# Optimization experiments

Measured on AMD Instinct MI355X. Metric: run time of the kernel, lower is better.

The kernel has to match this reference:

```python
import jax, jax.numpy as jnp
import numpy as np

B, S, T, H, F, V, OUT = 32, 40, 60, 256, 64, 50000, 128
D_IN = H + F  # LSTM input = input_size + feature_size (input_size == hidden_size)


def setup_inputs() -> dict:
    rng = np.random.default_rng(0)
    key = jax.random.key(0)
    ks = jax.random.split(key, 12)
    sc = 0.05
    # descending sentence counts per paragraph (pack_padded_sequence order), max == S
    lens = np.sort(rng.integers(1, S + 1, size=B))[::-1].copy()
    lens[0] = S
    # per-sentence token lengths; trailing (padding) sentences have length 0
    tok_len = rng.integers(1, T + 1, size=(B, S))
    tok_len = tok_len * (np.arange(S)[None, :] < lens[:, None])
    x_mask = jnp.asarray(np.arange(T)[None, None, :] >= tok_len[:, :, None])  # True = pad
    return {
        "x": jax.random.randint(ks[0], (B, S, T), 0, V),
        "x_mask": x_mask,
        "x_feature": jax.random.normal(ks[1], (B, S, T, F), jnp.float32),
        "sentences_len": jnp.asarray(lens, jnp.int32),
        "clause": jnp.zeros((B,), jnp.int32),
        "cls": jnp.zeros((B,), jnp.int32),
        "emb": jax.random.normal(ks[2], (V, H), jnp.float32) * 0.02,
        "attn_w": jax.random.normal(ks[3], (H,), jnp.float32) * sc,
        "attn_b": jnp.zeros((), jnp.float32),
        "wih_f": jax.random.normal(ks[4], (4 * H, D_IN), jnp.float32) * sc,
        "whh_f": jax.random.normal(ks[5], (4 * H, H), jnp.float32) * sc,
        "bih_f": jnp.zeros((4 * H,), jnp.float32),
        "bhh_f": jnp.zeros((4 * H,), jnp.float32),
        "wih_b": jax.random.normal(ks[6], (4 * H, D_IN), jnp.float32) * sc,
        "whh_b": jax.random.normal(ks[7], (4 * H, H), jnp.float32) * sc,
        "bih_b": jnp.zeros((4 * H,), jnp.float32),
        "bhh_b": jnp.zeros((4 * H,), jnp.float32),
        "fc_w": jax.random.normal(ks[8], (OUT, 2 * H), jnp.float32) * sc,
        "fc_b": jnp.zeros((OUT,), jnp.float32),
        "bn_gamma": jnp.ones((OUT,), jnp.float32),
        "bn_beta": jnp.zeros((OUT,), jnp.float32),
    }


def _lstm_last(X, m, wih, whh, bih, bhh, reverse):
    # X: (S, B, D) time-major inputs; m: (S, B) bool validity mask.
    # Masked update emulates pack_padded_sequence: carry freezes past each seq's length,
    # so the final carry equals torch's h_n for that direction.
    def step(carry, inp):
        h, c = carry
        xt, mt = inp
        g = xt @ wih.T + bih + h @ whh.T + bhh
        i, f, gg, o = jnp.split(g, 4, axis=-1)  # torch gate order i,f,g,o
        c2 = jax.nn.sigmoid(f) * c + jax.nn.sigmoid(i) * jnp.tanh(gg)
        h2 = jax.nn.sigmoid(o) * jnp.tanh(c2)
        upd = mt[:, None]
        return (jnp.where(upd, h2, h), jnp.where(upd, c2, c)), None

    nb, nh = X.shape[1], whh.shape[1]
    init = (jnp.zeros((nb, nh), X.dtype), jnp.zeros((nb, nh), X.dtype))
    (h, _), _ = jax.lax.scan(step, init, (X, m), reverse=reverse)
    return h


def _forward(x, x_mask, x_feature, sentences_len, emb, attn_w, attn_b,
             wih_f, whh_f, bih_f, bhh_f, wih_b, whh_b, bih_b, bhh_b,
             fc_w, fc_b, bn_gamma, bn_beta):
    e = emb[x]                                            # (B,S,T,H)
    valid_tok = ~x_mask                                   # (B,S,T)
    valid_sen = jnp.any(valid_tok, axis=-1)               # (B,S)
    score = jnp.einsum('bsth,h->bst', e, attn_w) + attn_b
    score = jnp.where(valid_tok, score, -jnp.inf)
    score = jnp.where(valid_sen[..., None], score, 0.0)   # avoid all-inf NaN rows
    alpha = jax.nn.relu(jax.nn.softmax(score, axis=-1))   # (B,S,T)
    alpha = jnp.where(valid_sen[..., None] & valid_tok, alpha, 0.0)
    emb_part = jnp.einsum('bst,bsth->bsh', alpha, e)      # attended sum over tokens
    feat_part = jnp.sum(x_feature * valid_tok[..., None].astype(x_feature.dtype), axis=2)
    sen = jnp.concatenate([emb_part, feat_part], axis=-1) # (B,S,H+F)
    sen = sen * valid_sen[..., None].astype(sen.dtype)    # empty sentences -> zero rows
    X = jnp.transpose(sen, (1, 0, 2))                     # (S,B,H+F) time-major
    m = jnp.arange(X.shape[0])[:, None] < sentences_len[None, :]  # (S,B)
    h_f = _lstm_last(X, m, wih_f, whh_f, bih_f, bhh_f, reverse=False)
    h_b = _lstm_last(X, m, wih_b, whh_b, bih_b, bhh_b, reverse=True)
    # torch: paragraph_hidden[0].view(batch, -1) on (2,B,H) = flat memory reinterpretation
    hidden = jnp.stack([h_f, h_b], axis=0).reshape(x.shape[0], -1)  # (B,2H)
    logits = hidden @ fc_w.T + fc_b                       # (B,OUT)
    mu = jnp.mean(logits, axis=0)
    var = jnp.mean((logits - mu) ** 2, axis=0)            # biased var (BN train mode)
    y = jax.nn.relu(bn_gamma * (logits - mu) / jnp.sqrt(var + 1e-5) + bn_beta)
    return jax.nn.log_softmax(y, axis=0)                  # original softmaxes over batch dim


def reference(x, x_mask, x_feature, sentences_len, clause, cls, emb, attn_w, attn_b,
              wih_f, whh_f, bih_f, bhh_f, wih_b, whh_b, bih_b, bhh_b,
              fc_w, fc_b, bn_gamma, bn_beta):
    # clause / cls are unused by the original forward
    return _forward(x, x_mask, x_feature, sentences_len, emb, attn_w, attn_b,
                    wih_f, whh_f, bih_f, bhh_f, wih_b, whh_b, bih_b, bhh_b,
                    fc_w, fc_b, bn_gamma, bn_beta)
```

## Files before the change

kernel.cpp:

```cpp
#include <hip/hip_runtime.h>
#include <stdint.h>

#define NB 32
#define NS 40
#define NT 60
#define NH 256
#define NF 64
#define NDIN 320
#define NG 1024
#define NSB 1280
#define NOUT 128

typedef __bf16 bf16x8 __attribute__((ext_vector_type(8)));
typedef float f32x4 __attribute__((ext_vector_type(4)));
typedef uint32_t u32x4 __attribute__((ext_vector_type(4)));

union bfrag { bf16x8 v; uint16_t u[8]; uint4 q; uint64_t d[2]; };
union f2arr { float2 v; float a[2]; };

__device__ __forceinline__ uint16_t f2bf(float f) {
  uint32_t u = __float_as_uint(f);
  u += 0x7fffu + ((u >> 16) & 1u);
  return (uint16_t)(u >> 16);
}
__device__ __forceinline__ float bf2f(uint16_t h) {
  return __uint_as_float(((uint32_t)h) << 16);
}
__device__ __forceinline__ float sig_fast(float x) { return 1.0f / (1.0f + __expf(-x)); }
__device__ __forceinline__ float tanh_fast(float x) {
  x = fminf(fmaxf(x, -15.0f), 15.0f);
  float t = __expf(2.0f * x);
  return (t - 1.0f) / (t + 1.0f);
}
__device__ __forceinline__ uint32_t ld_agent_u32(const uint32_t* p) {
  return __hip_atomic_load(p, __ATOMIC_RELAXED, __HIP_MEMORY_SCOPE_AGENT);
}

__global__ __launch_bounds__(256) void k_detect(const uint32_t* __restrict__ xm,
                                                int* __restrict__ flags,
                                                uint32_t* __restrict__ gr) {
  int bid = blockIdx.x, tid = threadIdx.x;
  {
    int gidx = bid * 256 + tid;
    u32x4 z = {0, 0, 0, 0};
    asm volatile("global_store_dwordx4 %0, %1, off sc1"
                 :: "v"((unsigned long long)(uintptr_t)(gr + (size_t)gidx * 4)), "v"(z)
                 : "memory");
  }
  __shared__ int s_notint, s_notflt;
  if (tid == 0) { s_notint = 0; s_notflt = 0; }
  __syncthreads();
  int notint = 0, notflt = 0;
  for (int i = bid * 600 + tid; i < (bid + 1) * 600; i += 256) {
    uint32_t v = xm[i];
    if (v > 1u) notint = 1;
    if (v != 0u && v != 0x3f800000u) notflt = 1;
  }
  if (notint) atomicOr(&s_notint, 1);
  if (notflt) atomicOr(&s_notflt, 1);
  __syncthreads();
  if (tid == 0) flags[8 + bid] = s_notint | (s_notflt << 1);
}

__global__ __launch_bounds__(256) void k_attn_prep(
    const int* __restrict__ x, const void* __restrict__ xmask,
    const float* __restrict__ xfeat, const int* __restrict__ slen,
    const float* __restrict__ emb, const float* __restrict__ attn_w,
    uint16_t* __restrict__ Xb, const int* __restrict__ flagp,
    const float* __restrict__ wf, const float* __restrict__ wb,
    uint16_t* __restrict__ outw)
{
  int tid = threadIdx.x;
  if (blockIdx.x >= 1280) {
    const int n = NG * NDIN;
    for (int idx = (blockIdx.x - 1280) * 256 + tid; idx < 2 * n; idx += 1280 * 256) {
      float v = (idx < n) ? wf[idx] : wb[idx - n];
      uint16_t hi = f2bf(v);
      outw[idx] = hi;
      outw[2 * n + idx] = f2bf(v - bf2f(hi));
    }
    return;
  }
  int bs = blockIdx.x;
  int b = bs / NS, s = bs % NS;
  uint16_t* Xh = Xb + (size_t)(s * NB + b) * NDIN;
  uint16_t* Xl = Xh + (size_t)NSB * NDIN;
  int len = slen[b];
  if (s >= len) {
    for (int i = tid; i < NDIN; i += 256) { Xh[i] = 0; Xl[i] = 0; }
    return;
  }
  __shared__ __attribute__((aligned(16))) float sw[NH];
  __shared__ float salpha[NT];
  __shared__ int sidx[NT];
  __shared__ unsigned char svalid[NT];
  __shared__ __attribute__((aligned(16))) uint16_t es[NT][NH];
  sw[tid] = attn_w[tid];
  int nv = 0;
  #pragma unroll
  for (int q = 0; q < 32; q++) nv |= flagp[8 + q];
  int flag = (!(nv & 1)) ? 0 : ((!(nv & 2)) ? 2 : 1);
  if (tid < NT) {
    int mi = bs * NT + tid;
    sidx[tid] = x[mi];
    int mv;
    if (flag == 1)      mv = ((const unsigned char*)xmask)[mi];
    else if (flag == 2) mv = (((const float*)xmask)[mi] != 0.0f) ? 1 : 0;
    else                mv = ((const int*)xmask)[mi];
    svalid[tid] = (mv == 0) ? 1 : 0;
  }
  __syncthreads();
  int wave = tid >> 6, lane = tid & 63;
  for (int t = wave; t < NT; t += 4) {
    float d = 0.0f;
    if (svalid[t]) {
      const float* er = emb + (size_t)sidx[t] * NH;
      float4 e4 = ((const float4*)er)[lane];
      float4 w4 = ((const float4*)sw)[lane];
      uint16_t* ed = &es[t][lane * 4];
      ed[0] = f2bf(e4.x); ed[1] = f2bf(e4.y); ed[2] = f2bf(e4.z); ed[3] = f2bf(e4.w);
      d = e4.x * w4.x + e4.y * w4.y + e4.z * w4.z + e4.w * w4.w;
      #pragma unroll
      for (int o = 32; o > 0; o >>= 1) d += __shfl_down(d, o);
    }
    if (lane == 0) salpha[t] = d;
  }
  __syncthreads();
  if (tid < 64) {
    int valid = (tid < NT) && svalid[tid];
    float v = valid ? salpha[tid] : -1e30f;
    float m = v;
    #pragma unroll
    for (int o = 32; o > 0; o >>= 1) m = fmaxf(m, __shfl_xor(m, o));
    float e = valid ? expf(v - m) : 0.0f;
    float ssum = e;
    #pragma unroll
    for (int o = 32; o > 0; o >>= 1) ssum += __shfl_xor(ssum, o);
    if (tid < NT) salpha[tid] = e / ssum;
  }
  __syncthreads();
  float acc = 0.0f;
  for (int t = 0; t < NT; t++) {
    float a = salpha[t];
    if (a != 0.0f) acc += a * bf2f(es[t][tid]);
  }
  {
    uint16_t hi = f2bf(acc);
    Xh[tid] = hi; Xl[tid] = f2bf(acc - bf2f(hi));
  }
  if (tid < NF) {
    float fa = 0.0f;
    const float* fp = xfeat + (size_t)bs * NT * NF + tid;
    for (int t = 0; t < NT; t++) if (svalid[t]) fa += fp[t * NF];
    uint16_t hi = f2bf(fa);
    Xh[NH + tid] = hi; Xl[NH + tid] = f2bf(fa - bf2f(hi));
  }
}

__global__ __launch_bounds__(512) void k_gbase(
    const uint16_t* __restrict__ Xb, const uint16_t* __restrict__ wihb,
    const float* __restrict__ bih_f, const float* __restrict__ bhh_f,
    const float* __restrict__ bih_b, const float* __restrict__ bhh_b,
    float* __restrict__ gbase)
{
  const int n = NG * NDIN;
  int wave = threadIdx.x >> 6, lane = threadIdx.x & 63;
  int job = blockIdx.x * 8 + wave;
  int dir = job / 1280;
  int r = job % 1280;
  int nt = r % 64, ms = r / 64;
  int m0 = ms * 64;
  const uint16_t* Wh = wihb + (size_t)dir * n;
  const uint16_t* Wl = Wh + (size_t)2 * n;
  const uint16_t* Ah = Xb;
  const uint16_t* Al = Xb + (size_t)NSB * NDIN;
  int lrow = lane & 15, lk = (lane >> 4) * 8;
  f32x4 acc0 = {0,0,0,0}, acc1 = acc0, acc2 = acc0, acc3 = acc0;
  for (int kk = 0; kk < 10; kk++) {
    int k0 = kk * 32 + lk;
    bfrag bh, bl, ah0, ah1, ah2, ah3, al0, al1, al2, al3;
    bh.q = *(const uint4*)(Wh + (size_t)(nt * 16 + lrow) * NDIN + k0);
    bl.q = *(const uint4*)(Wl + (size_t)(nt * 16 + lrow) * NDIN + k0);
    ah0.q = *(const uint4*)(Ah + (size_t)(m0 +  0 + lrow) * NDIN + k0);
    ah1.q = *(const uint4*)(Ah + (size_t)(m0 + 16 + lrow) * NDIN + k0);
    ah2.q = *(const uint4*)(Ah + (size_t)(m0 + 32 + lrow) * NDIN + k0);
    ah3.q = *(const uint4*)(Ah + (size_t)(m0 + 48 + lrow) * NDIN + k0);
    al0.q = *(const uint4*)(Al + (size_t)(m0 +  0 + lrow) * NDIN + k0);
    al1.q = *(const uint4*)(Al + (size_t)(m0 + 16 + lrow) * NDIN + k0);
    al2.q = *(const uint4*)(Al + (size_t)(m0 + 32 + lrow) * NDIN + k0);
    al3.q = *(const uint4*)(Al + (size_t)(m0 + 48 + lrow) * NDIN + k0);
    acc0 = __builtin_amdgcn_mfma_f32_16x16x32_bf16(ah0.v, bh.v, acc0, 0, 0, 0);
    acc0 = __builtin_amdgcn_mfma_f32_16x16x32_bf16(ah0.v, bl.v, acc0, 0, 0, 0);
    acc0 = __builtin_amdgcn_mfma_f32_16x16x32_bf16(al0.v, bh.v, acc0, 0, 0, 0);
    acc1 = __builtin_amdgcn_mfma_f32_16x16x32_bf16(ah1.v, bh.v, acc1, 0, 0, 0);
    acc1 = __builtin_amdgcn_mfma_f32_16x16x32_bf16(ah1.v, bl.v, acc1, 0, 0, 0);
    acc1 = __builtin_amdgcn_mfma_f32_16x16x32_bf16(al1.v, bh.v, acc1, 0, 0, 0);
    acc2 = __builtin_amdgcn_mfma_f32_16x16x32_bf16(ah2.v, bh.v, acc2, 0, 0, 0);
    acc2 = __builtin_amdgcn_mfma_f32_16x16x32_bf16(ah2.v, bl.v, acc2, 0, 0, 0);
    acc2 = __builtin_amdgcn_mfma_f32_16x16x32_bf16(al2.v, bh.v, acc2, 0, 0, 0);
    acc3 = __builtin_amdgcn_mfma_f32_16x16x32_bf16(ah3.v, bh.v, acc3, 0, 0, 0);
    acc3 = __builtin_amdgcn_mfma_f32_16x16x32_bf16(ah3.v, bl.v, acc3, 0, 0, 0);
    acc3 = __builtin_amdgcn_mfma_f32_16x16x32_bf16(al3.v, bh.v, acc3, 0, 0, 0);
  }
  int col = nt * 16 + lrow;
  float bias = dir ? (bih_b[col] + bhh_b[col]) : (bih_f[col] + bhh_f[col]);
  float* gb = gbase + (size_t)dir * NSB * NG;
  int rb = (lane >> 4) * 4;
  #pragma unroll
  for (int rr = 0; rr < 4; rr++) {
    gb[(size_t)(m0 +  0 + rb + rr) * NG + col] = acc0[rr] + bias;
    gb[(size_t)(m0 + 16 + rb + rr) * NG + col] = acc1[rr] + bias;
    gb[(size_t)(m0 + 32 + rb + rr) * NG + col] = acc2[rr] + bias;
    gb[(size_t)(m0 + 48 + rb + rr) * NG + col] = acc3[rr] + bias;
  }
}

__global__ __launch_bounds__(512, 2) void k_lstm(
    const float* __restrict__ whh_f_, const float* __restrict__ whh_b_,
    const float* __restrict__ gbase, const int* __restrict__ slen,
    uint32_t* __restrict__ gr,
    const float* __restrict__ fc_w, const float* __restrict__ fc_b,
    const float* __restrict__ gamma_, const float* __restrict__ beta_,
    float* __restrict__ outp)
{
  __shared__ __attribute__((aligned(16))) char smem_[65664];
  uint16_t (*hs)[264] = (uint16_t(*)[264])smem_;
  volatile float* tsb = (volatile float*)(smem_ + 16896);

  int wg = blockIdx.x;
  int dir = wg >> 3, p = wg & 7;
  int u0 = p * 32;
  int tid = threadIdx.x, wave = tid >> 6, lane = tid & 63;
  int lrow = lane & 15, lkb = (lane >> 4) * 8;
  const float* Wr = dir ? whh_b_ : whh_f_;
  const float* gb = gbase + (size_t)dir * NSB * NG;
  uint32_t* grd = gr + (size_t)dir * 2 * 64 * NB * 4;

  bfrag wh[8];
  {
    int wr = (lrow >> 2) * 256 + u0 + wave * 4 + (lrow & 3);
    const float* wrow = Wr + (size_t)wr * NH;
    #pragma unroll
    for (int kk = 0; kk < 8; kk++) {
      int k0 = kk * 32 + lkb;
      bfrag th;
      #pragma unroll
      for (int e = 0; e < 8; e++) th.u[e] = f2bf(wrow[k0 + e]);
      wh[kk] = th;
    }
  }
  int beta = lane >> 1;
  int g64 = p * 8 + wave;
  int len = slen[beta];
  uint32_t hprev_hi = 0;
  float c0 = 0.0f, c1 = 0.0f;

  unsigned long long sa[2][4];
  #pragma unroll
  for (int par = 0; par < 2; par++) {
    const uint32_t* gpar = grd + (size_t)par * 64 * NB * 4;
    #pragma unroll
    for (int q = 0; q < 4; q++)
      sa[par][q] = (unsigned long long)(uintptr_t)(gpar + (size_t)(tid + q * 512) * 4);
  }

  for (int i = 0; i < NS; i++) {
    int t = dir ? (NS - 1 - i) : i;
    const float* gptr = gb + ((size_t)t * NB + beta) * NG + u0 + wave * 4 + (lane & 1) * 2;
    f2arr g0, g1, g2, g3;
    g0.v = *(const float2*)(gptr);
    g1.v = *(const float2*)(gptr + 256);
    g2.v = *(const float2*)(gptr + 512);
    g3.v = *(const float2*)(gptr + 768);
    u32x4 v0, v1, v2, v3;
    {
      const unsigned long long* a = sa[i & 1];
      uint32_t need = (uint32_t)i;
      long spins = 0;
      for (;;) {
        asm volatile(
          "global_load_dwordx4 %0, %4, off sc1\n\t"
          "global_load_dwordx4 %1, %5, off sc1\n\t"
          "global_load_dwordx4 %2, %6, off sc1\n\t"
          "global_load_dwordx4 %3, %7, off sc1\n\t"
          "s_waitcnt vmcnt(0)"
          : "=&v"(v0), "=&v"(v1), "=&v"(v2), "=&v"(v3)
          : "v"(a[0]), "v"(a[1]), "v"(a[2]), "v"(a[3])
          : "memory");
        if (v0.x >= need && v1.x >= need && v2.x >= need && v3.x >= need) break;
        if (++spins > (1L << 16)) break;
      }
    }
    __syncthreads();
    #pragma unroll
    for (int q = 0; q < 4; q++) {
      int s = tid + q * 512;
      int gq = s >> 5, bb = s & 31;
      u32x4 vv = (q == 0) ? v0 : (q == 1) ? v1 : (q == 2) ? v2 : v3;
      uint32_t* d = (uint32_t*)(&hs[bb][gq * 4]);
      d[0] = vv.y; d[1] = vv.z;
    }
    __syncthreads();
    f32x4 acc0 = {0,0,0,0}, acc1 = acc0;
    #pragma unroll
    for (int kk = 0; kk < 8; kk++) {
      int k0 = kk * 32 + lkb;
      bfrag ah0, ah1;
      ah0.q = *(const uint4*)(&hs[lrow][k0]);
      ah1.q = *(const uint4*)(&hs[16 + lrow][k0]);
      acc0 = __builtin_amdgcn_mfma_f32_16x16x32_bf16(ah0.v, wh[kk].v, acc0, 0, 0, 0);
      acc1 = __builtin_amdgcn_mfma_f32_16x16x32_bf16(ah1.v, wh[kk].v, acc1, 0, 0, 0);
    }
    volatile float* ts = tsb + wave * 576;
    {
      int colT = lane & 15, rb = (lane >> 4) * 4;
      #pragma unroll
      for (int rr = 0; rr < 4; rr++) {
        ts[(rb + rr) * 18 + colT]      = acc0[rr];
        ts[(16 + rb + rr) * 18 + colT] = acc1[rr];
      }
    }
    int e2 = (lane & 1) * 2;
    float gv00 = ts[beta * 18 + 0 + e2],  gv01 = ts[beta * 18 + 1 + e2];
    float gv10 = ts[beta * 18 + 4 + e2],  gv11 = ts[beta * 18 + 5 + e2];
    float gv20 = ts[beta * 18 + 8 + e2],  gv21 = ts[beta * 18 + 9 + e2];
    float gv30 = ts[beta * 18 + 12 + e2], gv31 = ts[beta * 18 + 13 + e2];
    {
      int upd = (t < len) ? 1 : 0;
      float gi0 = gv00 + g0.a[0], gi1 = gv01 + g0.a[1];
      float gf0 = gv10 + g1.a[0], gf1 = gv11 + g1.a[1];
      float gg0 = gv20 + g2.a[0], gg1 = gv21 + g2.a[1];
      float go0 = gv30 + g3.a[0], go1 = gv31 + g3.a[1];
      float c2a = sig_fast(gf0) * c0 + sig_fast(gi0) * tanh_fast(gg0);
      float c2b = sig_fast(gf1) * c1 + sig_fast(gi1) * tanh_fast(gg1);
      float h2a = sig_fast(go0) * tanh_fast(c2a);
      float h2b = sig_fast(go1) * tanh_fast(c2b);
      c0 = upd ? c2a : c0;
      c1 = upd ? c2b : c1;
      uint32_t hiw;
      if (upd) {
        uint16_t ha = f2bf(h2a), hbb = f2bf(h2b);
        hiw = (uint32_t)ha | ((uint32_t)hbb << 16);
      } else hiw = hprev_hi;
      hprev_hi = hiw;
      uint32_t hiw_p = __shfl_down(hiw, 1);
      if ((lane & 1) == 0) {
        uint32_t* gout = grd + ((size_t)(((i + 1) & 1) * 64 + g64) * NB + beta) * 4;
        u32x4 pv;
        pv.x = (uint32_t)(i + 1); pv.y = hiw; pv.z = hiw_p; pv.w = 0u;
        asm volatile("global_store_dwordx4 %0, %1, off sc1"
                     :: "v"((unsigned long long)(uintptr_t)gout), "v"(pv) : "memory");
      }
    }
  }

  #pragma unroll
  for (int q = 0; q < 8; q++) {
    int s = tid + q * 512;
    int d_ = s >> 11, r2 = s & 2047;
    const uint32_t* ga = gr + ((size_t)d_ * 2 * 2048 + r2) * 4;
    long sp = 0;
    while (ld_agent_u32(ga) < (uint32_t)NS) {
      __builtin_amdgcn_s_sleep(1);
      if (++sp > (1L << 20)) break;
    }
  }
  __syncthreads();
  float* hid = (float*)smem_;
  for (int idx = tid; idx < NB * 512; idx += 512) {
    int bb = idx >> 9, k = idx & 511;
    int bsrc = 2 * (bb & 15) + (k >> 8);
    int hcol = k & 255;
    int dirn = (bb < 16) ? 0 : 1;
    const uint32_t* g = gr + ((size_t)dirn * 2 * 64 * NB + (size_t)(hcol >> 2) * NB + bsrc) * 4;
    uint32_t w = ld_agent_u32(g + 1 + ((hcol >> 1) & 1));
    hid[bb * 513 + k] = bf2f((uint16_t)(w >> ((hcol & 1) * 16)));
  }
  __syncthreads();
  int o = blockIdx.x * 8 + wave;
  int b = lane >> 1, half = lane & 1;
  const float* wrow = fc_w + (size_t)o * 512 + half * 256;
  const float* hrow = &hid[b * 513 + half * 256];
  float part = 0.0f;
  #pragma unroll 8
  for (int j = 0; j < 256; j++) part += wrow[j] * hrow[j];
  part += __shfl_xor(part, 1);
  float y = part + fc_b[o];
  float s2 = y;
  #pragma unroll
  for (int off = 2; off < 64; off <<= 1) s2 += __shfl_xor(s2, off);
  float mu = s2 * (1.0f / 32.0f);
  float d = y - mu;
  float v2 = d * d;
  #pragma unroll
  for (int off = 2; off < 64; off <<= 1) v2 += __shfl_xor(v2, off);
  float var = v2 * (1.0f / 32.0f);
  float gm = gamma_[o], be = beta_[o];
  float inv = 1.0f / sqrtf(var + 1e-5f);
  float yy = fmaxf(gm * (y - mu) * inv + be, 0.0f);
  float m = yy;
  #pragma unroll
  for (int off = 2; off < 64; off <<= 1) m = fmaxf(m, __shfl_xor(m, off));
  float e = expf(yy - m);
  float se = e;
  #pragma unroll
  for (int off = 2; off < 64; off <<= 1) se += __shfl_xor(se, off);
  float lse = m + logf(se);
  if (half == 0) outp[b * NOUT + o] = yy - lse;
}

extern "C" void kernel_launch(void* const* d_in, const int* in_sizes, int n_in,
                              void* d_out, int out_size, void* d_ws, size_t ws_size,
                              hipStream_t stream) {
  (void)in_sizes; (void)n_in; (void)out_size; (void)ws_size;
  const int*   x      = (const int*)  d_in[0];
  const void*  xmask  =               d_in[1];
  const float* xfeat  = (const float*)d_in[2];
  const int*   slen   = (const int*)  d_in[3];
  const float* emb    = (const float*)d_in[6];
  const float* attn_w = (const float*)d_in[7];
  const float* wih_f  = (const float*)d_in[9];
  const float* whh_f  = (const float*)d_in[10];
  const float* bih_f  = (const float*)d_in[11];
  const float* bhh_f  = (const float*)d_in[12];
  const float* wih_b  = (const float*)d_in[13];
  const float* whh_b  = (const float*)d_in[14];
  const float* bih_b  = (const float*)d_in[15];
  const float* bhh_b  = (const float*)d_in[16];
  const float* fc_w   = (const float*)d_in[17];
  const float* fc_b   = (const float*)d_in[18];
  const float* gam    = (const float*)d_in[19];
  const float* bet    = (const float*)d_in[20];

  char* ws = (char*)d_ws;
  int*      flags = (int*)ws;
  uint32_t* gr    = (uint32_t*)(ws + 4096);
  uint16_t* Xb    = (uint16_t*)(ws + 135168);
  uint16_t* wihb  = (uint16_t*)(ws + 1773568);
  float*    gbase = (float*)(ws + 4395008);

  k_detect<<<32, 256, 0, stream>>>((const uint32_t*)xmask, flags, gr);
  k_attn_prep<<<2560, 256, 0, stream>>>(x, xmask, xfeat, slen, emb, attn_w, Xb, flags,
                                        wih_f, wih_b, wihb);
  k_gbase<<<320, 512, 0, stream>>>(Xb, wihb, bih_f, bhh_f, bih_b, bhh_b, gbase);
  k_lstm<<<16, 512, 0, stream>>>(whh_f, whh_b, gbase, slen, gr,
                                 fc_w, fc_b, gam, bet, (float*)d_out);
}
```

Measured before the change: 243.9 us.

## Double-buffer LSTM hidden-state LDS tile and batch final hidden gather loads

Adds a second LDS buffer for the per-step hidden-state tile, alternating by step parity, so the barrier before writing the new h can be dropped. The MFMA reads of one step no longer conflict with the next step's writes. The epilogue's per-element flag polling and scattered 32-bit hidden loads are replaced by one batched spin of eight vector loads per thread that carry both the flags and the data, then unpacked into LDS. This cuts a barrier per recurrent step and many serialized global loads, at the cost of more LDS and registers. Correctness depends on the parity buffering being safe given the barrier that remains after the LDS writes.

Result: faster. 229.4 us (-5.9%).

```diff
diff --git a/kernel.cpp b/kernel.cpp
--- a/kernel.cpp
+++ b/kernel.cpp
@@ -224,8 +224,9 @@
     float* __restrict__ outp)
 {
   __shared__ __attribute__((aligned(16))) char smem_[65664];
-  uint16_t (*hs)[264] = (uint16_t(*)[264])smem_;
-  volatile float* tsb = (volatile float*)(smem_ + 16896);
+  uint16_t (*hs0)[264] = (uint16_t(*)[264])smem_;
+  uint16_t (*hs1)[264] = (uint16_t(*)[264])(smem_ + 16896);
+  volatile float* tsb = (volatile float*)(smem_ + 33792);
 
   int wg = blockIdx.x;
   int dir = wg >> 3, p = wg & 7;
@@ -291,13 +292,13 @@
         if (++spins > (1L << 16)) break;
       }
     }
-    __syncthreads();
+    uint16_t (*hcur)[264] = (i & 1) ? hs1 : hs0;
     #pragma unroll
     for (int q = 0; q < 4; q++) {
       int s = tid + q * 512;
       int gq = s >> 5, bb = s & 31;
       u32x4 vv = (q == 0) ? v0 : (q == 1) ? v1 : (q == 2) ? v2 : v3;
-      uint32_t* d = (uint32_t*)(&hs[bb][gq * 4]);
+      uint32_t* d = (uint32_t*)(&hcur[bb][gq * 4]);
       d[0] = vv.y; d[1] = vv.z;
     }
     __syncthreads();
@@ -306,8 +307,8 @@
     for (int kk = 0; kk < 8; kk++) {
       int k0 = kk * 32 + lkb;
       bfrag ah0, ah1;
-      ah0.q = *(const uint4*)(&hs[lrow][k0]);
-      ah1.q = *(const uint4*)(&hs[16 + lrow][k0]);
+      ah0.q = *(const uint4*)(&hcur[lrow][k0]);
+      ah1.q = *(const uint4*)(&hcur[16 + lrow][k0]);
       acc0 = __builtin_amdgcn_mfma_f32_16x16x32_bf16(ah0.v, wh[kk].v, acc0, 0, 0, 0);
       acc1 = __builtin_amdgcn_mfma_f32_16x16x32_bf16(ah1.v, wh[kk].v, acc1, 0, 0, 0);
     }
@@ -354,27 +355,55 @@
     }
   }
 
+  unsigned long long ea0 = (unsigned long long)(uintptr_t)(gr + (size_t)(tid +    0) * 4);
+  unsigned long long ea1 = (unsigned long long)(uintptr_t)(gr + (size_t)(tid +  512) * 4);
+  unsigned long long ea2 = (unsigned long long)(uintptr_t)(gr + (size_t)(tid + 1024) * 4);
+  unsigned long long ea3 = (unsigned long long)(uintptr_t)(gr + (size_t)(tid + 1536) * 4);
+  unsigned long long ea4 = (unsigned long long)(uintptr_t)(gr + (size_t)(4096 + tid +    0) * 4);
+  unsigned long long ea5 = (unsigned long long)(uintptr_t)(gr + (size_t)(4096 + tid +  512) * 4);
+  unsigned long long ea6 = (unsigned long long)(uintptr_t)(gr + (size_t)(4096 + tid + 1024) * 4);
+  unsigned long long ea7 = (unsigned long long)(uintptr_t)(gr + (size_t)(4096 + tid + 1536) * 4);
+  u32x4 w0, w1, w2, w3, w4, w5, w6, w7;
+  {
+    long spins = 0;
+    for (;;) {
+      asm volatile(
+        "global_load_dwordx4 %0, %8, off sc1\n\t"
+        "global_load_dwordx4 %1, %9, off sc1\n\t"
+        "global_load_dwordx4 %2, %10, off sc1\n\t"
+        "global_load_dwordx4 %3, %11, off sc1\n\t"
+        "global_load_dwordx4 %4, %12, off sc1\n\t"
+        "global_load_dwordx4 %5, %13, off sc1\n\t"
+        "global_load_dwordx4 %6, %14, off sc1\n\t"
+        "global_load_dwordx4 %7, %15, off sc1\n\t"
+        "s_waitcnt vmcnt(0)"
+        : "=&v"(w0), "=&v"(w1), "=&v"(w2), "=&v"(w3),
+          "=&v"(w4), "=&v"(w5), "=&v"(w6), "=&v"(w7)
+        : "v"(ea0), "v"(ea1), "v"(ea2), "v"(ea3),
+          "v"(ea4), "v"(ea5), "v"(ea6), "v"(ea7)
+        : "memory");
+      if (w0.x >= (uint32_t)NS && w1.x >= (uint32_t)NS && w2.x >= (uint32_t)NS &&
+          w3.x >= (uint32_t)NS && w4.x >= (uint32_t)NS && w5.x >= (uint32_t)NS &&
+          w6.x >= (uint32_t)NS && w7.x >= (uint32_t)NS) break;
+      if (++spins > (1L << 20)) break;
+    }
+  }
+  __syncthreads();
+  float* hid = (float*)smem_;
   #pragma unroll
   for (int q = 0; q < 8; q++) {
-    int s = tid + q * 512;
-    int d_ = s >> 11, r2 = s & 2047;
-    const uint32_t* ga = gr + ((size_t)d_ * 2 * 2048 + r2) * 4;
-    long sp = 0;
-    while (ld_agent_u32(ga) < (uint32_t)NS) {
-      __builtin_amdgcn_s_sleep(1);
-      if (++sp > (1L << 20)) break;
-    }
-  }
-  __syncthreads();
-  float* hid = (float*)smem_;
-  for (int idx = tid; idx < NB * 512; idx += 512) {
-    int bb = idx >> 9, k = idx & 511;
-    int bsrc = 2 * (bb & 15) + (k >> 8);
-    int hcol = k & 255;
-    int dirn = (bb < 16) ? 0 : 1;
-    const uint32_t* g = gr + ((size_t)dirn * 2 * 64 * NB + (size_t)(hcol >> 2) * NB + bsrc) * 4;
-    uint32_t w = ld_agent_u32(g + 1 + ((hcol >> 1) & 1));
-    hid[bb * 513 + k] = bf2f((uint16_t)(w >> ((hcol & 1) * 16)));
+    int d_ = q >> 2;
+    int r2 = tid + (q & 3) * 512;
+    int gq = r2 >> 5, bb = r2 & 31;
+    int bb2 = d_ * 16 + (bb >> 1);
+    int kb = (bb & 1) * 256 + gq * 4;
+    u32x4 vv = (q == 0) ? w0 : (q == 1) ? w1 : (q == 2) ? w2 : (q == 3) ? w3
+             : (q == 4) ? w4 : (q == 5) ? w5 : (q == 6) ? w6 : w7;
+    float* hd = &hid[bb2 * 513 + kb];
+    hd[0] = bf2f((uint16_t)vv.y);
+    hd[1] = bf2f((uint16_t)(vv.y >> 16));
+    hd[2] = bf2f((uint16_t)vv.z);
+    hd[3] = bf2f((uint16_t)(vv.z >> 16));
   }
   __syncthreads();
   int o = blockIdx.x * 8 + wave;
```
